# Kernel tuning notes

Measured on AMD Instinct MI355X. Metric: run time of the kernel, lower is better.

The kernel has to match this reference:

```python
import jax, jax.numpy as jnp
import numpy as np
from jax import lax


def setup_inputs() -> dict:
    key = jax.random.key(0)
    ks = jax.random.split(key, 5)
    B, Cin, H, W = 16, 64, 64, 64
    HID, K = 128, 3
    x = jax.random.normal(ks[0], (B, Cin, H, W), jnp.float32)
    w_is = jax.random.normal(ks[1], (4 * HID, Cin, 1, K), jnp.float32) * 0.05
    b_is = jax.random.normal(ks[2], (4 * HID,), jnp.float32) * 0.05
    w_ss = jax.random.normal(ks[3], (4 * HID, HID, 1, K), jnp.float32) * 0.05
    b_ss = jax.random.normal(ks[4], (4 * HID,), jnp.float32) * 0.05
    return {"x": x, "w_is": w_is, "b_is": b_is, "w_ss": w_ss, "b_ss": b_ss}


def reference(x, w_is, b_is, w_ss, b_ss):
    # Shapes: x [B,Cin,H,W]; w_is [4h,Cin,1,k]; w_ss [4h,h,1,k]
    hid = w_ss.shape[1]
    k = w_is.shape[-1]
    pad = k // 2

    # MaskedConv2d mask type 'B' on a (1,k) kernel: keep center and left taps,
    # zero everything strictly right of center.
    mask = (jnp.arange(k) <= pad).astype(x.dtype)  # [k]
    w_is_m = w_is * mask[None, None, None, :]

    # Input-to-state conv over the whole image at once: [B,4h,H,W]
    z_is = lax.conv_general_dilated(
        x, w_is_m, window_strides=(1, 1), padding=[(0, 0), (pad, pad)]
    ) + b_is[None, :, None, None]

    # State-to-state conv is a 1D conv along W: kernel [4h, h, k]
    w1 = w_ss[:, :, 0, :]

    def step(carry, z_row):
        h, c = carry  # each [B, hid, W]
        z = z_row + lax.conv_general_dilated(
            h, w1, window_strides=(1,), padding=[(pad, pad)],
            dimension_numbers=("NCH", "OIH", "NCH"),
        ) + b_ss[None, :, None]
        i_g = jax.nn.sigmoid(z[:, :hid])
        f_g = jax.nn.sigmoid(z[:, hid:2 * hid])
        o_g = jax.nn.sigmoid(z[:, 2 * hid:3 * hid])
        g = jnp.tanh(z[:, 3 * hid:])
        c = f_g * c + i_g * g
        h = o_g * jnp.tanh(c)
        return (h, c), h

    B, _, H, W = x.shape
    h0 = jnp.zeros((B, hid, W), x.dtype)
    c0 = jnp.zeros((B, hid, W), x.dtype)
    zs = jnp.transpose(z_is, (2, 0, 1, 3))  # [H, B, 4h, W]
    _, hs = lax.scan(step, (h0, c0), zs)    # hs: [H, B, hid, W]
    return jnp.transpose(hs, (1, 2, 0, 3))  # [B, hid, H, W]
```

## Files before the change

kernel.cpp:

```cpp
#include <hip/hip_runtime.h>
#include <hip/hip_bf16.h>

#define B_    16
#define CIN   64
#define Hn    64
#define Wn    64
#define HID   128
#define SXS2  72
#define SHS   136
#define NJC   8
#define NBLK  (B_ * NJC)

typedef __attribute__((ext_vector_type(8))) short bfrag_t;
typedef __attribute__((ext_vector_type(4))) float f4_t;

#define HBUF_SHORTS (B_ * Wn * HID)
#define HBUF_BYTES  (HBUF_SHORTS * 2)
#define CNT_STRIDE  256

static __device__ __forceinline__ short f2bf(float f) {
    union { __hip_bfloat16 h; short s; } u;
    u.h = __float2bfloat16(f);
    return u.s;
}
static __device__ __forceinline__ float sigm(float z)  { return 1.f / (1.f + __expf(-z)); }
static __device__ __forceinline__ float tanhf_(float z){ return 2.f / (1.f + __expf(-2.f * z)) - 1.f; }

extern "C" __global__ __launch_bounds__(256, 1)
void rowlstm_kernel(const float* __restrict__ x,
                    const float* __restrict__ w_is,
                    const float* __restrict__ b_is,
                    const float* __restrict__ w_ss,
                    const float* __restrict__ b_ss,
                    float* __restrict__ out,
                    unsigned char* __restrict__ ws)
{
    const int tid  = threadIdx.x;
    const int bid  = blockIdx.x;
    const int b    = bid & 15;
    const int jc   = bid >> 4;
    const int lane = tid & 63;
    const int wv   = tid >> 6;
    const int l15  = lane & 15;
    const int quad = lane >> 4;

    short*    hbuf0 = (short*)ws;
    unsigned* cnt   = (unsigned*)(ws + 2 * HBUF_BYTES + b * CNT_STRIDE);

    __shared__ alignas(16) short sH[66 * SHS];
    __shared__ alignas(16) short sX2[65 * SXS2];

    bfrag_t a_frag[4][16];
    #pragma unroll
    for (int mt = 0; mt < 4; ++mt) {
        const int co = mt * HID + jc * 16 + l15;
        #pragma unroll
        for (int kt = 0; kt < 16; ++kt) {
            const int kk0 = kt * 32 + quad * 8;
            const float* p;
            if      (kt < 2)  p = &w_is[(co * CIN + kk0)         * 3 + 0];
            else if (kt < 4)  p = &w_is[(co * CIN + (kk0 - 64))  * 3 + 1];
            else if (kt < 8)  p = &w_ss[(co * HID + (kk0 - 128)) * 3 + 0];
            else if (kt < 12) p = &w_ss[(co * HID + (kk0 - 256)) * 3 + 1];
            else              p = &w_ss[(co * HID + (kk0 - 384)) * 3 + 2];
            bfrag_t v;
            #pragma unroll
            for (int j = 0; j < 8; ++j) v[j] = f2bf(p[j * 3]);
            a_frag[mt][kt] = v;
        }
    }

    float bias[4][4];
    #pragma unroll
    for (int g = 0; g < 4; ++g) {
        #pragma unroll
        for (int r = 0; r < 4; ++r) {
            const int co = g * HID + jc * 16 + quad * 4 + r;
            bias[g][r] = b_is[co] + b_ss[co];
        }
    }

    {
        bfrag_t z8 = {0,0,0,0,0,0,0,0};
        if (tid < 8)  *(bfrag_t*)&sX2[tid * 8] = z8;
        if (tid < 16) {
            *(bfrag_t*)&sH[tid * 8] = z8;
            *(bfrag_t*)&sH[65 * SHS + tid * 8] = z8;
        }
    }

    float creg[4] = {0.f, 0.f, 0.f, 0.f};
    const int wp  = wv * 16 + l15;

    const int xw  = tid & 63;
    const int xc2 = tid >> 6;
    float xr[16];
    #pragma unroll
    for (int e = 0; e < 16; ++e)
        xr[e] = x[((b * CIN + xc2 * 16 + e) * Hn + 0) * Wn + xw];

    const int cig = tid & 15;
    const int w0  = tid >> 4;

    for (int h = 0; h < Hn; ++h) {
        const short* rd_hb = hbuf0 + ((h & 1) ^ 1) * HBUF_SHORTS + b * Wn * HID;
        short*       wr_hb = hbuf0 + (h & 1) * HBUF_SHORTS + b * Wn * HID;

        if (h > 0) {
            const unsigned target = (unsigned)(NJC * h);
            while (__hip_atomic_load(cnt, __ATOMIC_RELAXED, __HIP_MEMORY_SCOPE_AGENT) < target)
                __builtin_amdgcn_s_sleep(1);
            asm volatile("" ::: "memory");
        }

        union { bfrag_t f; unsigned long long q[2]; } hu0, hu1, hu2, hu3;
        if (h > 0) {
            const unsigned long long* s0 = (const unsigned long long*)(rd_hb + (w0 +  0) * HID + cig * 8);
            const unsigned long long* s1 = (const unsigned long long*)(rd_hb + (w0 + 16) * HID + cig * 8);
            const unsigned long long* s2 = (const unsigned long long*)(rd_hb + (w0 + 32) * HID + cig * 8);
            const unsigned long long* s3 = (const unsigned long long*)(rd_hb + (w0 + 48) * HID + cig * 8);
            hu0.q[0] = __hip_atomic_load(s0,     __ATOMIC_RELAXED, __HIP_MEMORY_SCOPE_AGENT);
            hu0.q[1] = __hip_atomic_load(s0 + 1, __ATOMIC_RELAXED, __HIP_MEMORY_SCOPE_AGENT);
            hu1.q[0] = __hip_atomic_load(s1,     __ATOMIC_RELAXED, __HIP_MEMORY_SCOPE_AGENT);
            hu1.q[1] = __hip_atomic_load(s1 + 1, __ATOMIC_RELAXED, __HIP_MEMORY_SCOPE_AGENT);
            hu2.q[0] = __hip_atomic_load(s2,     __ATOMIC_RELAXED, __HIP_MEMORY_SCOPE_AGENT);
            hu2.q[1] = __hip_atomic_load(s2 + 1, __ATOMIC_RELAXED, __HIP_MEMORY_SCOPE_AGENT);
            hu3.q[0] = __hip_atomic_load(s3,     __ATOMIC_RELAXED, __HIP_MEMORY_SCOPE_AGENT);
            hu3.q[1] = __hip_atomic_load(s3 + 1, __ATOMIC_RELAXED, __HIP_MEMORY_SCOPE_AGENT);
        } else {
            hu0.q[0] = hu0.q[1] = 0ull; hu1.q[0] = hu1.q[1] = 0ull;
            hu2.q[0] = hu2.q[1] = 0ull; hu3.q[0] = hu3.q[1] = 0ull;
        }

        {
            bfrag_t v0, v1;
            #pragma unroll
            for (int e = 0; e < 8; ++e) { v0[e] = f2bf(xr[e]); v1[e] = f2bf(xr[e + 8]); }
            *(bfrag_t*)&sX2[(xw + 1) * SXS2 + xc2 * 16]     = v0;
            *(bfrag_t*)&sX2[(xw + 1) * SXS2 + xc2 * 16 + 8] = v1;
        }
        {
            const int hp = (h < Hn - 1) ? h + 1 : h;
            #pragma unroll
            for (int e = 0; e < 16; ++e)
                xr[e] = x[((b * CIN + xc2 * 16 + e) * Hn + hp) * Wn + xw];
        }
        *(bfrag_t*)&sH[(w0 +  1) * SHS + cig * 8] = hu0.f;
        *(bfrag_t*)&sH[(w0 + 17) * SHS + cig * 8] = hu1.f;
        *(bfrag_t*)&sH[(w0 + 33) * SHS + cig * 8] = hu2.f;
        *(bfrag_t*)&sH[(w0 + 49) * SHS + cig * 8] = hu3.f;

        __syncthreads();

        f4_t acc0 = {0.f,0.f,0.f,0.f}, acc1 = {0.f,0.f,0.f,0.f};
        f4_t acc2 = {0.f,0.f,0.f,0.f}, acc3 = {0.f,0.f,0.f,0.f};
        #pragma unroll
        for (int kt = 0; kt < 16; ++kt) {
            const short* src;
            if (kt < 4) {
                src = &sX2[(wp + (kt >> 1)) * SXS2 + (kt & 1) * 32 + quad * 8];
            } else {
                src = &sH[(wp + ((kt - 4) >> 2)) * SHS + ((kt - 4) & 3) * 32 + quad * 8];
            }
            bfrag_t bf = *(const bfrag_t*)src;
            acc0 = __builtin_amdgcn_mfma_f32_16x16x32_bf16(a_frag[0][kt], bf, acc0, 0, 0, 0);
            acc1 = __builtin_amdgcn_mfma_f32_16x16x32_bf16(a_frag[1][kt], bf, acc1, 0, 0, 0);
            acc2 = __builtin_amdgcn_mfma_f32_16x16x32_bf16(a_frag[2][kt], bf, acc2, 0, 0, 0);
            acc3 = __builtin_amdgcn_mfma_f32_16x16x32_bf16(a_frag[3][kt], bf, acc3, 0, 0, 0);
        }

        float hv[4];
        #pragma unroll
        for (int r = 0; r < 4; ++r) {
            float ig = sigm (acc0[r] + bias[0][r]);
            float fg = sigm (acc1[r] + bias[1][r]);
            float og = sigm (acc2[r] + bias[2][r]);
            float gg = tanhf_(acc3[r] + bias[3][r]);
            float c  = fg * creg[r] + ig * gg;
            creg[r]  = c;
            hv[r]    = og * tanhf_(c);
            out[((b * HID + jc * 16 + quad * 4 + r) * Hn + h) * Wn + wp] = hv[r];
        }
        {
            unsigned p0 = (unsigned)(unsigned short)f2bf(hv[0]) |
                          ((unsigned)(unsigned short)f2bf(hv[1]) << 16);
            unsigned p1 = (unsigned)(unsigned short)f2bf(hv[2]) |
                          ((unsigned)(unsigned short)f2bf(hv[3]) << 16);
            unsigned long long pk = (unsigned long long)p0 | ((unsigned long long)p1 << 32);
            unsigned long long* dst = (unsigned long long*)(wr_hb + wp * HID + jc * 16 + quad * 4);
            __hip_atomic_store(dst, pk, __ATOMIC_RELAXED, __HIP_MEMORY_SCOPE_AGENT);
        }

        __syncthreads();

        if (h < Hn - 1 && tid == 0)
            __hip_atomic_fetch_add(cnt, 1u, __ATOMIC_RELAXED, __HIP_MEMORY_SCOPE_AGENT);
    }
}

extern "C" void kernel_launch(void* const* d_in, const int* in_sizes, int n_in,
                              void* d_out, int out_size, void* d_ws, size_t ws_size,
                              hipStream_t stream) {
    const float* x    = (const float*)d_in[0];
    const float* w_is = (const float*)d_in[1];
    const float* b_is = (const float*)d_in[2];
    const float* w_ss = (const float*)d_in[3];
    const float* b_ss = (const float*)d_in[4];
    float* out = (float*)d_out;
    unsigned char* ws = (unsigned char*)d_ws;

    hipMemsetAsync(ws + 2 * HBUF_BYTES, 0, B_ * CNT_STRIDE, stream);

    rowlstm_kernel<<<dim3(NBLK), dim3(256), 0, stream>>>(x, w_is, b_is, w_ss, b_ss, out, ws);
}
```

Baseline: 310.7 us.

## Replace counter barrier with self-validating fp16 h-state flags and split x/h MFMAs

Drops the per-batch atomic counter. The h-state is now stored as fp16 with an offset of +2 and a sign that alternates every two rows, so a reader can tell from the value whether the data is fresh and polls only the words it still needs. The offset is undone through a precomputed weight-sum bias correction, and the pad columns are filled with the encoded zero. Operands switch from bf16 to fp16. The input-to-state MFMAs are issued before the wait so they overlap with the poll, and the x prefetch moves after the store. The risks are fp16 precision loss from the +2 offset and correctness relying on the encoded value range.

```diff
diff --git a/kernel.cpp b/kernel.cpp
--- a/kernel.cpp
+++ b/kernel.cpp
@@ -11,20 +11,20 @@
 #define NJC   8
 #define NBLK  (B_ * NJC)
 
-typedef __attribute__((ext_vector_type(8))) short bfrag_t;
+typedef _Float16 h8_t __attribute__((ext_vector_type(8)));
 typedef __attribute__((ext_vector_type(4))) float f4_t;
 
 #define HBUF_SHORTS (B_ * Wn * HID)
 #define HBUF_BYTES  (HBUF_SHORTS * 2)
-#define CNT_STRIDE  256
-
-static __device__ __forceinline__ short f2bf(float f) {
-    union { __hip_bfloat16 h; short s; } u;
-    u.h = __float2bfloat16(f);
-    return u.s;
-}
+
 static __device__ __forceinline__ float sigm(float z)  { return 1.f / (1.f + __expf(-z)); }
 static __device__ __forceinline__ float tanhf_(float z){ return 2.f / (1.f + __expf(-2.f * z)) - 1.f; }
+
+#define BAR_LGKM() do { \
+    asm volatile("s_waitcnt lgkmcnt(0)" ::: "memory"); \
+    __builtin_amdgcn_s_barrier(); \
+    __builtin_amdgcn_sched_barrier(0); \
+} while (0)
 
 extern "C" __global__ __launch_bounds__(256, 1)
 void rowlstm_kernel(const float* __restrict__ x,
@@ -44,13 +44,13 @@
     const int l15  = lane & 15;
     const int quad = lane >> 4;
 
-    short*    hbuf0 = (short*)ws;
-    unsigned* cnt   = (unsigned*)(ws + 2 * HBUF_BYTES + b * CNT_STRIDE);
+    short* hbuf0 = (short*)ws;
 
     __shared__ alignas(16) short sH[66 * SHS];
     __shared__ alignas(16) short sX2[65 * SXS2];
-
-    bfrag_t a_frag[4][16];
+    __shared__ float sS3[4][16];
+
+    h8_t a_frag[4][16];
     #pragma unroll
     for (int mt = 0; mt < 4; ++mt) {
         const int co = mt * HID + jc * 16 + l15;
@@ -63,29 +63,39 @@
             else if (kt < 8)  p = &w_ss[(co * HID + (kk0 - 128)) * 3 + 0];
             else if (kt < 12) p = &w_ss[(co * HID + (kk0 - 256)) * 3 + 1];
             else              p = &w_ss[(co * HID + (kk0 - 384)) * 3 + 2];
-            bfrag_t v;
-            #pragma unroll
-            for (int j = 0; j < 8; ++j) v[j] = f2bf(p[j * 3]);
+            h8_t v;
+            #pragma unroll
+            for (int j = 0; j < 8; ++j) v[j] = (_Float16)p[j * 3];
             a_frag[mt][kt] = v;
         }
     }
 
-    float bias[4][4];
+    #pragma unroll
+    for (int mt = 0; mt < 4; ++mt) {
+        float s = 0.f;
+        #pragma unroll
+        for (int kt = 4; kt < 16; ++kt) {
+            #pragma unroll
+            for (int j = 0; j < 8; ++j) s += (float)a_frag[mt][kt][j];
+        }
+        s += __shfl_xor(s, 16);
+        s += __shfl_xor(s, 32);
+        if (wv == 0 && quad == 0) sS3[mt][l15] = s;
+    }
+
+    {
+        h8_t z8 = {0,0,0,0,0,0,0,0};
+        if (tid < 8) *(h8_t*)&sX2[tid * 8] = z8;
+    }
+    __syncthreads();
+
+    float bias2[4][4];
     #pragma unroll
     for (int g = 0; g < 4; ++g) {
         #pragma unroll
         for (int r = 0; r < 4; ++r) {
             const int co = g * HID + jc * 16 + quad * 4 + r;
-            bias[g][r] = b_is[co] + b_ss[co];
-        }
-    }
-
-    {
-        bfrag_t z8 = {0,0,0,0,0,0,0,0};
-        if (tid < 8)  *(bfrag_t*)&sX2[tid * 8] = z8;
-        if (tid < 16) {
-            *(bfrag_t*)&sH[tid * 8] = z8;
-            *(bfrag_t*)&sH[65 * SHS + tid * 8] = z8;
+            bias2[g][r] = b_is[co] + b_ss[co] - 2.f * sS3[g][quad * 4 + r];
         }
     }
 
@@ -103,98 +113,142 @@
     const int w0  = tid >> 4;
 
     for (int h = 0; h < Hn; ++h) {
+        const int p_read  = (h > 0) ? (((h - 1) >> 1) & 1) : 0;
+        const int p_store = (h >> 1) & 1;
+        const unsigned short psign = (unsigned short)(p_read << 15);
+
         const short* rd_hb = hbuf0 + ((h & 1) ^ 1) * HBUF_SHORTS + b * Wn * HID;
         short*       wr_hb = hbuf0 + (h & 1) * HBUF_SHORTS + b * Wn * HID;
 
+        {
+            const unsigned long long g = p_read ? 0xC000C000C000C000ULL : 0x4000400040004000ULL;
+            if (tid < 16) {
+                *(unsigned long long*)&sH[tid * 8]     = g;
+                *(unsigned long long*)&sH[tid * 8 + 4] = g;
+            } else if (tid < 32) {
+                const int t = tid - 16;
+                *(unsigned long long*)&sH[65 * SHS + t * 8]     = g;
+                *(unsigned long long*)&sH[65 * SHS + t * 8 + 4] = g;
+            }
+        }
+
+        unsigned long long qv[8];
+        unsigned need = 0;
         if (h > 0) {
-            const unsigned target = (unsigned)(NJC * h);
-            while (__hip_atomic_load(cnt, __ATOMIC_RELAXED, __HIP_MEMORY_SCOPE_AGENT) < target)
-                __builtin_amdgcn_s_sleep(1);
-            asm volatile("" ::: "memory");
-        }
-
-        union { bfrag_t f; unsigned long long q[2]; } hu0, hu1, hu2, hu3;
-        if (h > 0) {
-            const unsigned long long* s0 = (const unsigned long long*)(rd_hb + (w0 +  0) * HID + cig * 8);
-            const unsigned long long* s1 = (const unsigned long long*)(rd_hb + (w0 + 16) * HID + cig * 8);
-            const unsigned long long* s2 = (const unsigned long long*)(rd_hb + (w0 + 32) * HID + cig * 8);
-            const unsigned long long* s3 = (const unsigned long long*)(rd_hb + (w0 + 48) * HID + cig * 8);
-            hu0.q[0] = __hip_atomic_load(s0,     __ATOMIC_RELAXED, __HIP_MEMORY_SCOPE_AGENT);
-            hu0.q[1] = __hip_atomic_load(s0 + 1, __ATOMIC_RELAXED, __HIP_MEMORY_SCOPE_AGENT);
-            hu1.q[0] = __hip_atomic_load(s1,     __ATOMIC_RELAXED, __HIP_MEMORY_SCOPE_AGENT);
-            hu1.q[1] = __hip_atomic_load(s1 + 1, __ATOMIC_RELAXED, __HIP_MEMORY_SCOPE_AGENT);
-            hu2.q[0] = __hip_atomic_load(s2,     __ATOMIC_RELAXED, __HIP_MEMORY_SCOPE_AGENT);
-            hu2.q[1] = __hip_atomic_load(s2 + 1, __ATOMIC_RELAXED, __HIP_MEMORY_SCOPE_AGENT);
-            hu3.q[0] = __hip_atomic_load(s3,     __ATOMIC_RELAXED, __HIP_MEMORY_SCOPE_AGENT);
-            hu3.q[1] = __hip_atomic_load(s3 + 1, __ATOMIC_RELAXED, __HIP_MEMORY_SCOPE_AGENT);
+            need = 0xFFu;
+            #pragma unroll
+            for (int it = 0; it < 8; ++it) {
+                const int w = w0 + (it >> 1) * 16;
+                qv[it] = __hip_atomic_load(
+                    (const unsigned long long*)(rd_hb + w * HID + cig * 8 + (it & 1) * 4),
+                    __ATOMIC_RELAXED, __HIP_MEMORY_SCOPE_AGENT);
+            }
         } else {
-            hu0.q[0] = hu0.q[1] = 0ull; hu1.q[0] = hu1.q[1] = 0ull;
-            hu2.q[0] = hu2.q[1] = 0ull; hu3.q[0] = hu3.q[1] = 0ull;
-        }
-
-        {
-            bfrag_t v0, v1;
-            #pragma unroll
-            for (int e = 0; e < 8; ++e) { v0[e] = f2bf(xr[e]); v1[e] = f2bf(xr[e + 8]); }
-            *(bfrag_t*)&sX2[(xw + 1) * SXS2 + xc2 * 16]     = v0;
-            *(bfrag_t*)&sX2[(xw + 1) * SXS2 + xc2 * 16 + 8] = v1;
-        }
-        {
-            const int hp = (h < Hn - 1) ? h + 1 : h;
-            #pragma unroll
-            for (int e = 0; e < 16; ++e)
-                xr[e] = x[((b * CIN + xc2 * 16 + e) * Hn + hp) * Wn + xw];
-        }
-        *(bfrag_t*)&sH[(w0 +  1) * SHS + cig * 8] = hu0.f;
-        *(bfrag_t*)&sH[(w0 + 17) * SHS + cig * 8] = hu1.f;
-        *(bfrag_t*)&sH[(w0 + 33) * SHS + cig * 8] = hu2.f;
-        *(bfrag_t*)&sH[(w0 + 49) * SHS + cig * 8] = hu3.f;
-
-        __syncthreads();
-
-        f4_t acc0 = {0.f,0.f,0.f,0.f}, acc1 = {0.f,0.f,0.f,0.f};
-        f4_t acc2 = {0.f,0.f,0.f,0.f}, acc3 = {0.f,0.f,0.f,0.f};
-        #pragma unroll
-        for (int kt = 0; kt < 16; ++kt) {
-            const short* src;
-            if (kt < 4) {
-                src = &sX2[(wp + (kt >> 1)) * SXS2 + (kt & 1) * 32 + quad * 8];
-            } else {
-                src = &sH[(wp + ((kt - 4) >> 2)) * SHS + ((kt - 4) & 3) * 32 + quad * 8];
-            }
-            bfrag_t bf = *(const bfrag_t*)src;
-            acc0 = __builtin_amdgcn_mfma_f32_16x16x32_bf16(a_frag[0][kt], bf, acc0, 0, 0, 0);
-            acc1 = __builtin_amdgcn_mfma_f32_16x16x32_bf16(a_frag[1][kt], bf, acc1, 0, 0, 0);
-            acc2 = __builtin_amdgcn_mfma_f32_16x16x32_bf16(a_frag[2][kt], bf, acc2, 0, 0, 0);
-            acc3 = __builtin_amdgcn_mfma_f32_16x16x32_bf16(a_frag[3][kt], bf, acc3, 0, 0, 0);
+            const unsigned long long fillv = 0x4000400040004000ULL;
+            #pragma unroll
+            for (int it = 0; it < 8; ++it) {
+                const int w = w0 + (it >> 1) * 16;
+                *(unsigned long long*)&sH[(w + 1) * SHS + cig * 8 + (it & 1) * 4] = fillv;
+            }
+        }
+
+        {
+            h8_t v0, v1;
+            #pragma unroll
+            for (int e = 0; e < 8; ++e) { v0[e] = (_Float16)xr[e]; v1[e] = (_Float16)xr[e + 8]; }
+            *(h8_t*)&sX2[(xw + 1) * SXS2 + xc2 * 16]     = v0;
+            *(h8_t*)&sX2[(xw + 1) * SXS2 + xc2 * 16 + 8] = v1;
+        }
+
+        BAR_LGKM();
+
+        f4_t ax0 = {0,0,0,0}, ax1 = {0,0,0,0}, ax2 = {0,0,0,0}, ax3 = {0,0,0,0};
+        #pragma unroll
+        for (int kt = 0; kt < 4; ++kt) {
+            const short* src = &sX2[(wp + (kt >> 1)) * SXS2 + (kt & 1) * 32 + quad * 8];
+            h8_t bf = *(const h8_t*)src;
+            ax0 = __builtin_amdgcn_mfma_f32_16x16x32_f16(a_frag[0][kt], bf, ax0, 0, 0, 0);
+            ax1 = __builtin_amdgcn_mfma_f32_16x16x32_f16(a_frag[1][kt], bf, ax1, 0, 0, 0);
+            ax2 = __builtin_amdgcn_mfma_f32_16x16x32_f16(a_frag[2][kt], bf, ax2, 0, 0, 0);
+            ax3 = __builtin_amdgcn_mfma_f32_16x16x32_f16(a_frag[3][kt], bf, ax3, 0, 0, 0);
+        }
+
+        while (need) {
+            #pragma unroll
+            for (int it = 0; it < 8; ++it) {
+                if (need & (1u << it)) {
+                    const unsigned long long q = qv[it];
+                    const unsigned short e = (unsigned short)q ^ psign;
+                    if (e >= 0x3C00u && e <= 0x4200u) {
+                        const int w = w0 + (it >> 1) * 16;
+                        *(unsigned long long*)&sH[(w + 1) * SHS + cig * 8 + (it & 1) * 4] = q;
+                        need &= ~(1u << it);
+                    }
+                }
+            }
+            if (!need) break;
+            __builtin_amdgcn_s_sleep(1);
+            #pragma unroll
+            for (int it = 0; it < 8; ++it) {
+                if (need & (1u << it)) {
+                    const int w = w0 + (it >> 1) * 16;
+                    qv[it] = __hip_atomic_load(
+                        (const unsigned long long*)(rd_hb + w * HID + cig * 8 + (it & 1) * 4),
+                        __ATOMIC_RELAXED, __HIP_MEMORY_SCOPE_AGENT);
+                }
+            }
+        }
+
+        BAR_LGKM();
+
+        f4_t ah0 = {0,0,0,0}, ah1 = {0,0,0,0}, ah2 = {0,0,0,0}, ah3 = {0,0,0,0};
+        #pragma unroll
+        for (int kt = 4; kt < 16; ++kt) {
+            const short* src = &sH[(wp + ((kt - 4) >> 2)) * SHS + ((kt - 4) & 3) * 32 + quad * 8];
+            h8_t bf = *(const h8_t*)src;
+            ah0 = __builtin_amdgcn_mfma_f32_16x16x32_f16(a_frag[0][kt], bf, ah0, 0, 0, 0);
+            ah1 = __builtin_amdgcn_mfma_f32_16x16x32_f16(a_frag[1][kt], bf, ah1, 0, 0, 0);
+            ah2 = __builtin_amdgcn_mfma_f32_16x16x32_f16(a_frag[2][kt], bf, ah2, 0, 0, 0);
+            ah3 = __builtin_amdgcn_mfma_f32_16x16x32_f16(a_frag[3][kt], bf, ah3, 0, 0, 0);
         }
 
         float hv[4];
         #pragma unroll
         for (int r = 0; r < 4; ++r) {
-            float ig = sigm (acc0[r] + bias[0][r]);
-            float fg = sigm (acc1[r] + bias[1][r]);
-            float og = sigm (acc2[r] + bias[2][r]);
-            float gg = tanhf_(acc3[r] + bias[3][r]);
+            const float h0v = p_read ? -ah0[r] : ah0[r];
+            const float h1v = p_read ? -ah1[r] : ah1[r];
+            const float h2v = p_read ? -ah2[r] : ah2[r];
+            const float h3v = p_read ? -ah3[r] : ah3[r];
+            float ig = sigm (ax0[r] + h0v + bias2[0][r]);
+            float fg = sigm (ax1[r] + h1v + bias2[1][r]);
+            float og = sigm (ax2[r] + h2v + bias2[2][r]);
+            float gg = tanhf_(ax3[r] + h3v + bias2[3][r]);
             float c  = fg * creg[r] + ig * gg;
             creg[r]  = c;
             hv[r]    = og * tanhf_(c);
             out[((b * HID + jc * 16 + quad * 4 + r) * Hn + h) * Wn + wp] = hv[r];
         }
         {
-            unsigned p0 = (unsigned)(unsigned short)f2bf(hv[0]) |
-                          ((unsigned)(unsigned short)f2bf(hv[1]) << 16);
-            unsigned p1 = (unsigned)(unsigned short)f2bf(hv[2]) |
-                          ((unsigned)(unsigned short)f2bf(hv[3]) << 16);
-            unsigned long long pk = (unsigned long long)p0 | ((unsigned long long)p1 << 32);
-            unsigned long long* dst = (unsigned long long*)(wr_hb + wp * HID + jc * 16 + quad * 4);
-            __hip_atomic_store(dst, pk, __ATOMIC_RELAXED, __HIP_MEMORY_SCOPE_AGENT);
-        }
-
-        __syncthreads();
-
-        if (h < Hn - 1 && tid == 0)
-            __hip_atomic_fetch_add(cnt, 1u, __ATOMIC_RELAXED, __HIP_MEMORY_SCOPE_AGENT);
+            unsigned long long pk = 0;
+            #pragma unroll
+            for (int r = 0; r < 4; ++r) {
+                float ef = hv[r] + 2.f;
+                if (p_store) ef = -ef;
+                union { _Float16 f; unsigned short s; } u;
+                u.f = (_Float16)ef;
+                pk |= ((unsigned long long)u.s) << (16 * r);
+            }
+            __hip_atomic_store((unsigned long long*)(wr_hb + wp * HID + jc * 16 + quad * 4),
+                               pk, __ATOMIC_RELAXED, __HIP_MEMORY_SCOPE_AGENT);
+        }
+        {
+            const int hp = (h < Hn - 1) ? h + 1 : h;
+            #pragma unroll
+            for (int e = 0; e < 16; ++e)
+                xr[e] = x[((b * CIN + xc2 * 16 + e) * Hn + hp) * Wn + xw];
+        }
+
+        BAR_LGKM();
     }
 }
 
@@ -209,7 +263,7 @@
     float* out = (float*)d_out;
     unsigned char* ws = (unsigned char*)d_ws;
 
-    hipMemsetAsync(ws + 2 * HBUF_BYTES, 0, B_ * CNT_STRIDE, stream);
+    hipMemsetAsync(ws, 0, 2 * HBUF_BYTES, stream);
 
     rowlstm_kernel<<<dim3(NBLK), dim3(256), 0, stream>>>(x, w_is, b_is, w_ss, b_ss, out, ws);
 }
```

Measured after the change: 429.3 us. 1.38x slower.

## Replace atomic counter with per-block flags and reorder row schedule around sync

Applied to the files above, without the earlier changes.

Replaces the shared fetch-add counter with per-column-block flag words that the producer block sets to the row index, polled by one wavefront with a ballot and no sleep. The x-part MFMAs are issued before the h-tile is written to LDS. The h handoff store and flag publish now come before the output store and next-row x prefetch, so the critical cross-block path is shorter. Lightweight barriers with explicit waitcnt replace __syncthreads. Busy polling without sleep may add memory traffic, and relaxed ordering relies on vmcnt waits for visibility.

```diff
diff --git a/kernel.cpp b/kernel.cpp
--- a/kernel.cpp
+++ b/kernel.cpp
@@ -16,7 +16,7 @@
 
 #define HBUF_SHORTS (B_ * Wn * HID)
 #define HBUF_BYTES  (HBUF_SHORTS * 2)
-#define CNT_STRIDE  256
+#define FLG_STRIDE  256
 
 static __device__ __forceinline__ short f2bf(float f) {
     union { __hip_bfloat16 h; short s; } u;
@@ -25,6 +25,18 @@
 }
 static __device__ __forceinline__ float sigm(float z)  { return 1.f / (1.f + __expf(-z)); }
 static __device__ __forceinline__ float tanhf_(float z){ return 2.f / (1.f + __expf(-2.f * z)) - 1.f; }
+
+#define BAR_LGKM() do { \
+    asm volatile("s_waitcnt lgkmcnt(0)" ::: "memory"); \
+    __builtin_amdgcn_s_barrier(); \
+    __builtin_amdgcn_sched_barrier(0); \
+} while (0)
+
+#define BAR_VM() do { \
+    asm volatile("s_waitcnt vmcnt(0)" ::: "memory"); \
+    __builtin_amdgcn_s_barrier(); \
+    __builtin_amdgcn_sched_barrier(0); \
+} while (0)
 
 extern "C" __global__ __launch_bounds__(256, 1)
 void rowlstm_kernel(const float* __restrict__ x,
@@ -45,7 +57,7 @@
     const int quad = lane >> 4;
 
     short*    hbuf0 = (short*)ws;
-    unsigned* cnt   = (unsigned*)(ws + 2 * HBUF_BYTES + b * CNT_STRIDE);
+    unsigned* flags = (unsigned*)(ws + 2 * HBUF_BYTES + b * FLG_STRIDE);
 
     __shared__ alignas(16) short sH[66 * SHS];
     __shared__ alignas(16) short sX2[65 * SXS2];
@@ -102,20 +114,26 @@
     const int cig = tid & 15;
     const int w0  = tid >> 4;
 
+    __syncthreads();
+
     for (int h = 0; h < Hn; ++h) {
         const short* rd_hb = hbuf0 + ((h & 1) ^ 1) * HBUF_SHORTS + b * Wn * HID;
         short*       wr_hb = hbuf0 + (h & 1) * HBUF_SHORTS + b * Wn * HID;
 
-        if (h > 0) {
-            const unsigned target = (unsigned)(NJC * h);
-            while (__hip_atomic_load(cnt, __ATOMIC_RELAXED, __HIP_MEMORY_SCOPE_AGENT) < target)
-                __builtin_amdgcn_s_sleep(1);
-            asm volatile("" ::: "memory");
-        }
+        if (h > 0 && wv == 0) {
+            const unsigned tgt = (unsigned)h;
+            for (;;) {
+                unsigned f = tgt;
+                if (lane < NJC)
+                    f = __hip_atomic_load(&flags[lane], __ATOMIC_RELAXED, __HIP_MEMORY_SCOPE_AGENT);
+                if (__all((int)(f >= tgt))) break;
+            }
+        }
+        BAR_LGKM();
 
         union { bfrag_t f; unsigned long long q[2]; } hu0, hu1, hu2, hu3;
         if (h > 0) {
-            const unsigned long long* s0 = (const unsigned long long*)(rd_hb + (w0 +  0) * HID + cig * 8);
+            const unsigned long long* s0 = (const unsigned long long*)(rd_hb + (w0     ) * HID + cig * 8);
             const unsigned long long* s1 = (const unsigned long long*)(rd_hb + (w0 + 16) * HID + cig * 8);
             const unsigned long long* s2 = (const unsigned long long*)(rd_hb + (w0 + 32) * HID + cig * 8);
             const unsigned long long* s3 = (const unsigned long long*)(rd_hb + (w0 + 48) * HID + cig * 8);
@@ -139,29 +157,29 @@
             *(bfrag_t*)&sX2[(xw + 1) * SXS2 + xc2 * 16]     = v0;
             *(bfrag_t*)&sX2[(xw + 1) * SXS2 + xc2 * 16 + 8] = v1;
         }
-        {
-            const int hp = (h < Hn - 1) ? h + 1 : h;
-            #pragma unroll
-            for (int e = 0; e < 16; ++e)
-                xr[e] = x[((b * CIN + xc2 * 16 + e) * Hn + hp) * Wn + xw];
-        }
+        BAR_LGKM();
+
+        f4_t acc0 = {0.f,0.f,0.f,0.f}, acc1 = {0.f,0.f,0.f,0.f};
+        f4_t acc2 = {0.f,0.f,0.f,0.f}, acc3 = {0.f,0.f,0.f,0.f};
+        #pragma unroll
+        for (int kt = 0; kt < 4; ++kt) {
+            const short* src = &sX2[(wp + (kt >> 1)) * SXS2 + (kt & 1) * 32 + quad * 8];
+            bfrag_t bf = *(const bfrag_t*)src;
+            acc0 = __builtin_amdgcn_mfma_f32_16x16x32_bf16(a_frag[0][kt], bf, acc0, 0, 0, 0);
+            acc1 = __builtin_amdgcn_mfma_f32_16x16x32_bf16(a_frag[1][kt], bf, acc1, 0, 0, 0);
+            acc2 = __builtin_amdgcn_mfma_f32_16x16x32_bf16(a_frag[2][kt], bf, acc2, 0, 0, 0);
+            acc3 = __builtin_amdgcn_mfma_f32_16x16x32_bf16(a_frag[3][kt], bf, acc3, 0, 0, 0);
+        }
+
         *(bfrag_t*)&sH[(w0 +  1) * SHS + cig * 8] = hu0.f;
         *(bfrag_t*)&sH[(w0 + 17) * SHS + cig * 8] = hu1.f;
         *(bfrag_t*)&sH[(w0 + 33) * SHS + cig * 8] = hu2.f;
         *(bfrag_t*)&sH[(w0 + 49) * SHS + cig * 8] = hu3.f;
-
-        __syncthreads();
-
-        f4_t acc0 = {0.f,0.f,0.f,0.f}, acc1 = {0.f,0.f,0.f,0.f};
-        f4_t acc2 = {0.f,0.f,0.f,0.f}, acc3 = {0.f,0.f,0.f,0.f};
-        #pragma unroll
-        for (int kt = 0; kt < 16; ++kt) {
-            const short* src;
-            if (kt < 4) {
-                src = &sX2[(wp + (kt >> 1)) * SXS2 + (kt & 1) * 32 + quad * 8];
-            } else {
-                src = &sH[(wp + ((kt - 4) >> 2)) * SHS + ((kt - 4) & 3) * 32 + quad * 8];
-            }
+        BAR_LGKM();
+
+        #pragma unroll
+        for (int kt = 4; kt < 16; ++kt) {
+            const short* src = &sH[(wp + ((kt - 4) >> 2)) * SHS + ((kt - 4) & 3) * 32 + quad * 8];
             bfrag_t bf = *(const bfrag_t*)src;
             acc0 = __builtin_amdgcn_mfma_f32_16x16x32_bf16(a_frag[0][kt], bf, acc0, 0, 0, 0);
             acc1 = __builtin_amdgcn_mfma_f32_16x16x32_bf16(a_frag[1][kt], bf, acc1, 0, 0, 0);
@@ -179,22 +197,31 @@
             float c  = fg * creg[r] + ig * gg;
             creg[r]  = c;
             hv[r]    = og * tanhf_(c);
-            out[((b * HID + jc * 16 + quad * 4 + r) * Hn + h) * Wn + wp] = hv[r];
-        }
-        {
+        }
+
+        if (h + 1 < Hn) {
             unsigned p0 = (unsigned)(unsigned short)f2bf(hv[0]) |
                           ((unsigned)(unsigned short)f2bf(hv[1]) << 16);
             unsigned p1 = (unsigned)(unsigned short)f2bf(hv[2]) |
                           ((unsigned)(unsigned short)f2bf(hv[3]) << 16);
             unsigned long long pk = (unsigned long long)p0 | ((unsigned long long)p1 << 32);
-            unsigned long long* dst = (unsigned long long*)(wr_hb + wp * HID + jc * 16 + quad * 4);
-            __hip_atomic_store(dst, pk, __ATOMIC_RELAXED, __HIP_MEMORY_SCOPE_AGENT);
-        }
-
-        __syncthreads();
-
-        if (h < Hn - 1 && tid == 0)
-            __hip_atomic_fetch_add(cnt, 1u, __ATOMIC_RELAXED, __HIP_MEMORY_SCOPE_AGENT);
+            __hip_atomic_store((unsigned long long*)(wr_hb + wp * HID + jc * 16 + quad * 4),
+                               pk, __ATOMIC_RELAXED, __HIP_MEMORY_SCOPE_AGENT);
+            BAR_VM();
+            if (tid == 0)
+                __hip_atomic_store(&flags[jc], (unsigned)(h + 1),
+                                   __ATOMIC_RELAXED, __HIP_MEMORY_SCOPE_AGENT);
+        }
+
+        #pragma unroll
+        for (int r = 0; r < 4; ++r)
+            out[((b * HID + jc * 16 + quad * 4 + r) * Hn + h) * Wn + wp] = hv[r];
+
+        if (h + 1 < Hn) {
+            #pragma unroll
+            for (int e = 0; e < 16; ++e)
+                xr[e] = x[((b * CIN + xc2 * 16 + e) * Hn + (h + 1)) * Wn + xw];
+        }
     }
 }
 
@@ -209,7 +236,7 @@
     float* out = (float*)d_out;
     unsigned char* ws = (unsigned char*)d_ws;
 
-    hipMemsetAsync(ws + 2 * HBUF_BYTES, 0, B_ * CNT_STRIDE, stream);
+    hipMemsetAsync(ws + 2 * HBUF_BYTES, 0, B_ * FLG_STRIDE, stream);
 
     rowlstm_kernel<<<dim3(NBLK), dim3(256), 0, stream>>>(x, w_is, b_is, w_ss, b_ss, out, ws);
 }
```

Measured after the change: 321.2 us. 1.03x slower.
